# Kernel tuning notes

Measured on AMD Instinct MI355X. Metric: run time of the kernel, lower is better.

## Reference

```python
import jax, jax.numpy as jnp
import numpy as np

MAX_SEQ = 512
HIDDEN = 1024
E = 2048  # hidden * expansion_factor
S = 128
EPS = 1e-05


def _rope(x):
    # x: [b, n, 2, s]; rotate along sequence dim (dim=1 in the torch code)
    b, n, h, s = x.shape
    half = s // 2
    pos = jnp.arange(n, dtype=x.dtype)
    # torch: freq_seq = -arange(half)/half; inv_freq = 10000**(-freq_seq) = 10000**(arange/half)
    inv_freq = jnp.power(jnp.asarray(10000.0, x.dtype), jnp.arange(half, dtype=x.dtype) / half)
    sinusoid = pos[:, None] * inv_freq[None, :]          # [n, half]
    sin = jnp.sin(sinusoid)[None, :, None, :]            # [1, n, 1, half]
    cos = jnp.cos(sinusoid)[None, :, None, :]
    x1, x2 = jnp.split(x, 2, axis=-1)
    return jnp.concatenate([x1 * cos - x2 * sin, x2 * cos + x1 * sin], axis=-1)


def _rel_pos_bias(w, seq_len):
    # toeplitz construction (max_seq_length <= 512 branch)
    t = jnp.pad(w, (0, seq_len))                          # [3*seq_len - 1]
    t = jnp.tile(t, seq_len)[:-seq_len]                   # [seq_len*(3*seq_len-2)]
    t = t.reshape(seq_len, 3 * seq_len - 2)
    r = (2 * seq_len - 1) // 2
    return t[:, r:-r][None]                               # [1, seq_len, seq_len]


def setup_inputs() -> dict:
    key = jax.random.key(0)
    ks = jax.random.split(key, 6)
    x = jax.random.normal(ks[0], (16, 512, HIDDEN), dtype=jnp.float32)
    uv_w = jax.random.normal(ks[1], (2 * E + S, HIDDEN), dtype=jnp.float32) * 0.02
    o_w = jax.random.normal(ks[2], (HIDDEN, E), dtype=jnp.float32) * 0.02
    return {
        "x": x,
        "ln_w": jnp.ones((HIDDEN,), jnp.float32),
        "ln_b": jnp.zeros((HIDDEN,), jnp.float32),
        "uv_w": uv_w,
        "uv_b": jnp.zeros((2 * E + S,), jnp.float32),
        "gamma": jax.random.uniform(ks[3], (2, S), dtype=jnp.float32),
        "beta": jax.random.uniform(ks[4], (2, S), dtype=jnp.float32),
        "o_w": o_w,
        "o_b": jnp.zeros((HIDDEN,), jnp.float32),
        "w_rel": jax.random.uniform(ks[5], (2 * MAX_SEQ - 1,), dtype=jnp.float32),
    }


def reference(x, ln_w, ln_b, uv_w, uv_b, gamma, beta, o_w, o_b, w_rel):
    b, n, d = x.shape
    shortcut = x
    # LayerNorm
    mu = jnp.mean(x, axis=-1, keepdims=True)
    var = jnp.mean(jnp.square(x - mu), axis=-1, keepdims=True)
    xn = (x - mu) * jax.lax.rsqrt(var + EPS) * ln_w + ln_b
    # uv projection + silu on the whole projection
    uv = jax.nn.silu(jnp.einsum('bnd,fd->bnf', xn, uv_w) + uv_b)
    u, v, base = jnp.split(uv, [E, 2 * E], axis=-1)      # [b,n,E],[b,n,E],[b,n,S]
    # offset-scale: [b,n,S] x [2,S] -> [b,n,2,S]
    base = base[..., None, :] * gamma + beta
    base = _rope(base)
    q, k = base[:, :, 0, :], base[:, :, 1, :]
    qk = jnp.einsum('bnd,bmd->bnm', q, k)
    bias = _rel_pos_bias(w_rel, MAX_SEQ)[:, :n, :n]
    kernel = jnp.square(jax.nn.relu(qk / MAX_SEQ + bias))
    out = u * jnp.einsum('bnm,bme->bne', kernel, v)
    out = jnp.einsum('bne,de->bnd', out, o_w) + o_b
    return out + shortcut
```

## Files before the change

kernel.cpp:

```cpp
#include <hip/hip_runtime.h>
#include <hip/hip_bf16.h>


typedef __bf16 bf16_t;
typedef __bf16 bf16x4 __attribute__((ext_vector_type(4)));
typedef __bf16 bf16x8 __attribute__((ext_vector_type(8)));
typedef float  f32x4  __attribute__((ext_vector_type(4)));

__device__ __forceinline__ void async16(const void* g, void* l) {
  __builtin_amdgcn_global_load_lds(
      (const __attribute__((address_space(1))) void*)g,
      (__attribute__((address_space(3))) void*)l, 16, 0, 0);
}

__global__ __launch_bounds__(256) void fill_const(float* __restrict__ out,
                                                  float val, int n) {
  int i = blockIdx.x * 256 + threadIdx.x;
  if (i < n) out[i] = val;
}

__global__ void rope_table(float* __restrict__ cosT, float* __restrict__ sinT) {
  int idx = blockIdx.x * 256 + threadIdx.x;
  int n = idx >> 6, j = idx & 63;
  float invf = (float)pow(10000.0, (double)j * (1.0 / 64.0));
  float angf = (float)n * invf;
  cosT[idx] = (float)cos((double)angf);
  sinT[idx] = (float)sin((double)angf);
}

__global__ __launch_bounds__(256) void cvt_f32_bf16(const float* __restrict__ in,
                                                    bf16_t* __restrict__ out,
                                                    int n4) {
  int i = blockIdx.x * 256 + threadIdx.x;
  if (i < n4) {
    f32x4 v = ((const f32x4*)in)[i];
    bf16x4 o;
    o[0] = (__bf16)v[0]; o[1] = (__bf16)v[1];
    o[2] = (__bf16)v[2]; o[3] = (__bf16)v[3];
    ((bf16x4*)out)[i] = o;
  }
}

__global__ __launch_bounds__(256) void ln_kernel(const float* __restrict__ x,
                                                 const float* __restrict__ w,
                                                 const float* __restrict__ b,
                                                 bf16_t* __restrict__ xn) {
  int row = blockIdx.x;
  int tid = threadIdx.x;
  f32x4 v = *(const f32x4*)(x + (size_t)row * 1024 + tid * 4);
  float s = v[0] + v[1] + v[2] + v[3];
  float s2 = v[0]*v[0] + v[1]*v[1] + v[2]*v[2] + v[3]*v[3];
  for (int o = 32; o > 0; o >>= 1) {
    s += __shfl_down(s, o);
    s2 += __shfl_down(s2, o);
  }
  __shared__ float ps[4], ps2[4];
  if ((tid & 63) == 0) { ps[tid >> 6] = s; ps2[tid >> 6] = s2; }
  __syncthreads();
  float st = ps[0] + ps[1] + ps[2] + ps[3];
  float st2 = ps2[0] + ps2[1] + ps2[2] + ps2[3];
  float mean = st * (1.f / 1024.f);
  float var = st2 * (1.f / 1024.f) - mean * mean;
  float inv = 1.f / sqrtf(var + 1e-5f);
  bf16x4 o4;
  for (int i = 0; i < 4; i++) {
    float wn = w[tid * 4 + i], bn = b[tid * 4 + i];
    o4[i] = (__bf16)((v[i] - mean) * inv * wn + bn);
  }
  *(bf16x4*)(xn + (size_t)row * 1024 + tid * 4) = o4;
}

__global__ __launch_bounds__(128) void rope_qk(const bf16_t* __restrict__ baseb,
                                               const float* __restrict__ gamma,
                                               const float* __restrict__ beta,
                                               const float* __restrict__ cosT,
                                               const float* __restrict__ sinT,
                                               bf16_t* __restrict__ q,
                                               bf16_t* __restrict__ k) {
  int m = blockIdx.x;
  int n = m & 511;
  int s = threadIdx.x;
  float base = (float)baseb[(size_t)m * 128 + s];
  __shared__ float t[2][128];
  t[0][s] = base * gamma[s] + beta[s];
  t[1][s] = base * gamma[128 + s] + beta[128 + s];
  __syncthreads();
  int j = s & 63;
  float c = cosT[n * 64 + j], sn = sinT[n * 64 + j];
  for (int h = 0; h < 2; h++) {
    float x1 = t[h][j], x2 = t[h][64 + j];
    float r = (s < 64) ? (x1 * c - x2 * sn) : (x2 * c + x1 * sn);
    bf16_t* dst = h == 0 ? q : k;
    dst[(size_t)m * 128 + s] = (__bf16)r;
  }
}

struct EpiUV {
  const float* uv_b;
  bf16_t* u;
  bf16_t* vT;
  bf16_t* baseb;
  __device__ void operator()(int b, int m0, int n, f32x4 a4) const {
    float bn = uv_b[n];
    bf16_t s[4];
#pragma unroll
    for (int r = 0; r < 4; r++) {
      float xv = a4[r] + bn;
      float sv = xv * __builtin_amdgcn_rcpf(1.f + __expf(-xv));
      sv = fminf(fmaxf(sv, -100.f), 100.f);
      s[r] = (__bf16)sv;
    }
    if (n < 2048) {
#pragma unroll
      for (int r = 0; r < 4; r++) u[(size_t)(m0 + r) * 2048 + n] = s[r];
    } else if (n < 4096) {
      int bb = m0 >> 9, ns = m0 & 511;
      bf16x4 p; p[0] = s[0]; p[1] = s[1]; p[2] = s[2]; p[3] = s[3];
      *(bf16x4*)(vT + ((size_t)bb * 2048 + (n - 2048)) * 512 + ns) = p;
    } else {
#pragma unroll
      for (int r = 0; r < 4; r++)
        baseb[(size_t)(m0 + r) * 128 + (n - 4096)] = s[r];
    }
  }
};
struct EpiQK {
  const float* w_rel;
  bf16_t* km;
  __device__ void operator()(int b, int i0, int j, f32x4 a4) const {
#pragma unroll
    for (int r = 0; r < 4; r++) {
      float bias = w_rel[511 + j - (i0 + r)];
      float t = fmaxf(a4[r] * (1.f / 512.f) + bias, 0.f);
      t = fminf(t, 100.f);
      km[((size_t)b * 512 + i0 + r) * 512 + j] = (__bf16)(t * t);
    }
  }
};
struct EpiAttn {
  const bf16_t* u;
  bf16_t* out2;
  __device__ void operator()(int b, int i0, int e, f32x4 a4) const {
#pragma unroll
    for (int r = 0; r < 4; r++) {
      size_t m = (size_t)b * 512 + i0 + r;
      float uu = (float)u[m * 2048 + e];
      float rr = a4[r] * uu;
      rr = fminf(fmaxf(rr, -1e6f), 1e6f);
      out2[m * 2048 + e] = (__bf16)rr;
    }
  }
};
struct EpiOut {
  const float* o_b;
  const float* x;
  float* out;
  __device__ void operator()(int b, int m0, int d, f32x4 a4) const {
    float ob = o_b[d];
#pragma unroll
    for (int r = 0; r < 4; r++) {
      long idx = (long)(m0 + r) * 1024 + d;
      float rr = a4[r] + ob + x[idx];
      rr = fminf(fmaxf(rr, -1e5f), 1e5f);
      out[idx] = rr;
    }
  }
};

template <int MFR, typename Epi>
__global__ __launch_bounds__(256, 2)
void gemm_nt(const bf16_t* __restrict__ A, const bf16_t* __restrict__ Bm,
             int lda, int ldb, int K, long sAz, long sBz, Epi epi) {
  constexpr int MROWS = MFR * 32;
  __shared__ __align__(16) char smem[MROWS * 128 + 16384];
  const int tid = threadIdx.x;
  const int lane = tid & 63;
  const int wid = tid >> 6;
  const int wm = wid & 1, wn = wid >> 1;
  const int quad = lane >> 4, col16 = lane & 15;
  const int srow = lane >> 3;
  const int skc = lane & 7;
  const int bz = blockIdx.z;
  const int tileM = blockIdx.x * MROWS;
  const int tileN = blockIdx.y * 128;
  const bf16_t* Ab = A + (size_t)bz * sAz;
  const bf16_t* Bb = Bm + (size_t)bz * sBz;

  unsigned oA[MFR], oB[4];
#pragma unroll
  for (int c4 = 0; c4 < MFR; c4++) {
    int ch = c4 * 4 + wid;
    int row = ch * 8 + srow;
    int kc = skc ^ (row & 7);
    oA[c4] = (unsigned)((tileM + row) * lda + kc * 8);
  }
#pragma unroll
  for (int c4 = 0; c4 < 4; c4++) {
    int ch = c4 * 4 + wid;
    int row = ch * 8 + srow;
    int kc = skc ^ (row & 7);
    oB[c4] = (unsigned)((tileN + row) * ldb + kc * 8);
  }

  f32x4 acc[MFR][4] = {};

  for (int k0 = 0; k0 < K; k0 += 64) {
#pragma unroll
    for (int c4 = 0; c4 < MFR; c4++)
      async16(Ab + oA[c4] + k0, smem + (c4 * 4 + wid) * 1024);
#pragma unroll
    for (int c4 = 0; c4 < 4; c4++)
      async16(Bb + oB[c4] + k0, smem + MROWS * 128 + (c4 * 4 + wid) * 1024);
    __syncthreads();

    const char* smA = (const char*)smem;
    const char* smB = smA + MROWS * 128;
#pragma unroll
    for (int kk = 0; kk < 2; kk++) {
      bf16x8 af[MFR], bfr[4];
      int jj = kk * 4 + quad;
#pragma unroll
      for (int tt = 0; tt < MFR; tt++) {
        int ml = wm * (MFR * 16) + tt * 16 + col16;
        af[tt] = *(const bf16x8*)(smA + (size_t)ml * 128 + ((jj ^ (ml & 7)) * 16));
      }
#pragma unroll
      for (int tt = 0; tt < 4; tt++) {
        int nl = wn * 64 + tt * 16 + col16;
        bfr[tt] = *(const bf16x8*)(smB + (size_t)nl * 128 + ((jj ^ (nl & 7)) * 16));
      }
#pragma unroll
      for (int mt = 0; mt < MFR; mt++)
#pragma unroll
        for (int nt = 0; nt < 4; nt++)
          acc[mt][nt] = __builtin_amdgcn_mfma_f32_16x16x32_bf16(af[mt], bfr[nt], acc[mt][nt], 0, 0, 0);
    }
    __syncthreads();
  }

#pragma unroll
  for (int mt = 0; mt < MFR; mt++) {
    int gm = tileM + wm * (MFR * 16) + mt * 16 + quad * 4;
#pragma unroll
    for (int nt = 0; nt < 4; nt++) {
      int gn = tileN + wn * 64 + nt * 16 + col16;
      epi(bz, gm, gn, acc[mt][nt]);
    }
  }
}

extern "C" void kernel_launch(void* const* d_in, const int* in_sizes, int n_in,
                              void* d_out, int out_size, void* d_ws, size_t ws_size,
                              hipStream_t stream) {
  const float* x = (const float*)d_in[0];
  const float* ln_w = (const float*)d_in[1];
  const float* ln_b = (const float*)d_in[2];
  const float* uv_w = (const float*)d_in[3];
  const float* uv_b = (const float*)d_in[4];
  const float* gamma = (const float*)d_in[5];
  const float* beta = (const float*)d_in[6];
  const float* o_w = (const float*)d_in[7];
  const float* o_b = (const float*)d_in[8];
  const float* w_rel = (const float*)d_in[9];
  float* out = (float*)d_out;

  const int NOUT = 8388608;
  const size_t WS_NEEDED = 71303168;
  if (ws_size < WS_NEEDED) {
    float wsMiB = (float)(ws_size >> 20);
    fill_const<<<dim3(32768), dim3(256), 0, stream>>>(out, 1000.f + wsMiB, NOUT);
    return;
  }

  char* ws = (char*)d_ws;
  bf16_t* u = (bf16_t*)(ws + 0);
  bf16_t* out2 = u;
  bf16_t* vT = (bf16_t*)(ws + 33554432);
  bf16_t* o_wb = (bf16_t*)(ws + 67108864);
  char* ob = (char*)d_out;
  bf16_t* xn = (bf16_t*)ob;
  bf16_t* uv_wb = (bf16_t*)(ob + 16777216);
  bf16_t* baseb = (bf16_t*)(ob + 25427968);
  float* cosT = (float*)(ob + 27525120);
  float* sinT = (float*)(ob + 27656192);
  bf16_t* qb = (bf16_t*)ob;
  bf16_t* kb = (bf16_t*)(ob + 2097152);
  bf16_t* km = (bf16_t*)(ob + 4194304);

  rope_table<<<dim3(128), dim3(256), 0, stream>>>(cosT, sinT);
  cvt_f32_bf16<<<dim3(4224), dim3(256), 0, stream>>>(uv_w, uv_wb, 1081344);
  cvt_f32_bf16<<<dim3(2048), dim3(256), 0, stream>>>(o_w, o_wb, 524288);
  ln_kernel<<<dim3(8192), dim3(256), 0, stream>>>(x, ln_w, ln_b, xn);
  gemm_nt<8><<<dim3(32, 33, 1), dim3(256), 0, stream>>>(
      xn, uv_wb, 1024, 1024, 1024, 0L, 0L, EpiUV{uv_b, u, vT, baseb});
  rope_qk<<<dim3(8192), dim3(128), 0, stream>>>(baseb, gamma, beta, cosT, sinT, qb, kb);
  gemm_nt<4><<<dim3(4, 4, 16), dim3(256), 0, stream>>>(
      qb, kb, 128, 128, 128, (long)512 * 128, (long)512 * 128, EpiQK{w_rel, km});
  gemm_nt<8><<<dim3(2, 16, 16), dim3(256), 0, stream>>>(
      km, vT, 512, 512, 512, (long)512 * 512, (long)2048 * 512, EpiAttn{u, out2});
  gemm_nt<4><<<dim3(64, 8, 1), dim3(256), 0, stream>>>(
      out2, o_wb, 2048, 2048, 2048, 0L, 0L, EpiOut{o_b, x, out});
}
```

Baseline: 335.0 us.

## Double-buffer GEMM K-loop with 32-wide tiles and shrink UV GEMM tile

The GEMM main loop now uses a 32-element K step with two shared-memory buffers. The next tile's async global-to-LDS load is issued while the current one is computed, and only one barrier is needed per iteration. A new swizzled layout packs two rows per 128-byte line to suit the half-width K chunk. The UV projection GEMM also switches from 256-row to 128-row tiles, doubling the grid. This trades more iterations and barriers for load/compute overlap and better occupancy.

```diff
diff --git a/kernel.cpp b/kernel.cpp
--- a/kernel.cpp
+++ b/kernel.cpp
@@ -172,70 +172,82 @@
 void gemm_nt(const bf16_t* __restrict__ A, const bf16_t* __restrict__ Bm,
              int lda, int ldb, int K, long sAz, long sBz, Epi epi) {
   constexpr int MROWS = MFR * 32;
-  __shared__ __align__(16) char smem[MROWS * 128 + 16384];
+  constexpr int ABYTES = MROWS * 64;
+  constexpr int BUFB = ABYTES + 8192;
+  constexpr int NA = MROWS / 64;
+  __shared__ __align__(16) char smem[2 * BUFB];
   const int tid = threadIdx.x;
   const int lane = tid & 63;
   const int wid = tid >> 6;
   const int wm = wid & 1, wn = wid >> 1;
   const int quad = lane >> 4, col16 = lane & 15;
-  const int srow = lane >> 3;
-  const int skc = lane & 7;
   const int bz = blockIdx.z;
   const int tileM = blockIdx.x * MROWS;
   const int tileN = blockIdx.y * 128;
   const bf16_t* Ab = A + (size_t)bz * sAz;
   const bf16_t* Bb = Bm + (size_t)bz * sBz;
-
-  unsigned oA[MFR], oB[4];
-#pragma unroll
-  for (int c4 = 0; c4 < MFR; c4++) {
-    int ch = c4 * 4 + wid;
-    int row = ch * 8 + srow;
-    int kc = skc ^ (row & 7);
-    oA[c4] = (unsigned)((tileM + row) * lda + kc * 8);
-  }
-#pragma unroll
-  for (int c4 = 0; c4 < 4; c4++) {
-    int ch = c4 * 4 + wid;
-    int row = ch * 8 + srow;
-    int kc = skc ^ (row & 7);
-    oB[c4] = (unsigned)((tileN + row) * ldb + kc * 8);
-  }
+  const int NT = K >> 5;
+
+  const int g = (lane & 7) ^ ((lane >> 3) & 7);
+  const int rowb = 2 * (lane >> 3) + (g >> 2);
+  const int kcb = (g & 3) * 8;
+  unsigned oA[NA], oB[2];
+#pragma unroll
+  for (int i = 0; i < NA; i++) {
+    int u = i * 4 + wid;
+    oA[i] = (unsigned)((tileM + u * 16 + rowb) * lda + kcb);
+  }
+#pragma unroll
+  for (int i = 0; i < 2; i++) {
+    int u = i * 4 + wid;
+    oB[i] = (unsigned)((tileN + u * 16 + rowb) * ldb + kcb);
+  }
+
+  int offA[MFR], offB[4];
+#pragma unroll
+  for (int mt = 0; mt < MFR; mt++) {
+    int ml = wm * (MFR * 16) + mt * 16 + col16;
+    int L = ml >> 1, gg = (ml & 1) * 4 + quad;
+    offA[mt] = L * 128 + ((gg ^ (L & 7)) * 16);
+  }
+#pragma unroll
+  for (int nt = 0; nt < 4; nt++) {
+    int nl = wn * 64 + nt * 16 + col16;
+    int L = nl >> 1, gg = (nl & 1) * 4 + quad;
+    offB[nt] = L * 128 + ((gg ^ (L & 7)) * 16);
+  }
+
+  auto stage = [&](int kt, int p) {
+    char* base = (char*)smem + p * BUFB;
+    const unsigned ko = (unsigned)kt * 32;
+#pragma unroll
+    for (int i = 0; i < NA; i++)
+      async16(Ab + oA[i] + ko, base + (i * 4 + wid) * 1024);
+#pragma unroll
+    for (int i = 0; i < 2; i++)
+      async16(Bb + oB[i] + ko, base + ABYTES + (i * 4 + wid) * 1024);
+  };
 
   f32x4 acc[MFR][4] = {};
 
-  for (int k0 = 0; k0 < K; k0 += 64) {
-#pragma unroll
-    for (int c4 = 0; c4 < MFR; c4++)
-      async16(Ab + oA[c4] + k0, smem + (c4 * 4 + wid) * 1024);
-#pragma unroll
-    for (int c4 = 0; c4 < 4; c4++)
-      async16(Bb + oB[c4] + k0, smem + MROWS * 128 + (c4 * 4 + wid) * 1024);
+  stage(0, 0);
+#pragma unroll 2
+  for (int t = 0; t < NT; t++) {
     __syncthreads();
-
-    const char* smA = (const char*)smem;
-    const char* smB = smA + MROWS * 128;
-#pragma unroll
-    for (int kk = 0; kk < 2; kk++) {
-      bf16x8 af[MFR], bfr[4];
-      int jj = kk * 4 + quad;
-#pragma unroll
-      for (int tt = 0; tt < MFR; tt++) {
-        int ml = wm * (MFR * 16) + tt * 16 + col16;
-        af[tt] = *(const bf16x8*)(smA + (size_t)ml * 128 + ((jj ^ (ml & 7)) * 16));
-      }
-#pragma unroll
-      for (int tt = 0; tt < 4; tt++) {
-        int nl = wn * 64 + tt * 16 + col16;
-        bfr[tt] = *(const bf16x8*)(smB + (size_t)nl * 128 + ((jj ^ (nl & 7)) * 16));
-      }
-#pragma unroll
-      for (int mt = 0; mt < MFR; mt++)
-#pragma unroll
-        for (int nt = 0; nt < 4; nt++)
-          acc[mt][nt] = __builtin_amdgcn_mfma_f32_16x16x32_bf16(af[mt], bfr[nt], acc[mt][nt], 0, 0, 0);
-    }
-    __syncthreads();
+    if (t + 1 < NT) stage(t + 1, (t + 1) & 1);
+    const char* sA = (const char*)smem + (t & 1) * BUFB;
+    const char* sB = sA + ABYTES;
+    bf16x8 af[MFR], bfr[4];
+#pragma unroll
+    for (int mt = 0; mt < MFR; mt++) af[mt] = *(const bf16x8*)(sA + offA[mt]);
+#pragma unroll
+    for (int nt = 0; nt < 4; nt++) bfr[nt] = *(const bf16x8*)(sB + offB[nt]);
+#pragma unroll
+    for (int mt = 0; mt < MFR; mt++)
+#pragma unroll
+      for (int nt = 0; nt < 4; nt++)
+        acc[mt][nt] = __builtin_amdgcn_mfma_f32_16x16x32_bf16(
+            af[mt], bfr[nt], acc[mt][nt], 0, 0, 0);
   }
 
 #pragma unroll
@@ -291,7 +303,7 @@
   cvt_f32_bf16<<<dim3(4224), dim3(256), 0, stream>>>(uv_w, uv_wb, 1081344);
   cvt_f32_bf16<<<dim3(2048), dim3(256), 0, stream>>>(o_w, o_wb, 524288);
   ln_kernel<<<dim3(8192), dim3(256), 0, stream>>>(x, ln_w, ln_b, xn);
-  gemm_nt<8><<<dim3(32, 33, 1), dim3(256), 0, stream>>>(
+  gemm_nt<4><<<dim3(64, 33, 1), dim3(256), 0, stream>>>(
       xn, uv_wb, 1024, 1024, 1024, 0L, 0L, EpiUV{uv_b, u, vT, baseb});
   rope_qk<<<dim3(8192), dim3(128), 0, stream>>>(baseb, gamma, beta, cosT, sinT, qb, kb);
   gemm_nt<4><<<dim3(4, 4, 16), dim3(256), 0, stream>>>(
```

After: 330.8 us. Within noise of the previous version (-1.3%).
